# Optimization experiments

Measured on AMD Instinct MI355X. Metric: run time of the kernel, lower is better.

The kernel has to match this reference:

```python
import jax, jax.numpy as jnp
import numpy as np

B, IC, HC = 262144, 128, 128


def setup_inputs() -> dict:
    key = jax.random.key(0)
    ks = jax.random.split(key, 12)
    s_ih = 1.0 / np.sqrt(IC)
    s_hh = 1.0 / np.sqrt(HC)
    return {
        "x": jax.random.normal(ks[0], (B, IC), jnp.float32),
        "u": jax.random.uniform(ks[1], (B, 1), jnp.float32),
        "h": jax.random.normal(ks[2], (B, HC), jnp.float32) * 0.1,
        "c": jax.random.normal(ks[3], (B, HC), jnp.float32) * 0.1,
        "delta_u": jax.random.uniform(ks[4], (B, 1), jnp.float32),
        "skip": jax.random.randint(ks[5], (B,), 0, 2) == 1,
        # LSTMCell params (PyTorch gate order: i, f, g, o)
        "W_ih": jax.random.normal(ks[6], (4 * HC, IC), jnp.float32) * s_ih,
        "W_hh": jax.random.normal(ks[7], (4 * HC, HC), jnp.float32) * s_hh,
        "b_ih": jnp.zeros((4 * HC,), jnp.float32),
        "b_hh": jnp.zeros((4 * HC,), jnp.float32),
        # Linear(hc -> 1), bias initialized to 1 per the module
        "lin_w": jax.random.normal(ks[8], (1, HC), jnp.float32) * s_hh,
        "lin_b": jnp.ones((1,), jnp.float32),
    }


def _ste_round(u):
    # straight-through estimator: forward round, identity backward
    return u + jax.lax.stop_gradient(jnp.round(u) - u)


def reference(x, u, h, c, delta_u, skip, W_ih, W_hh, b_ih, b_hh, lin_w, lin_b):
    bu = _ste_round(u)  # [B,1]

    # --- no-skip branch: LSTM cell + update-gate linear ---
    gates = x @ W_ih.T + b_ih + h @ W_hh.T + b_hh  # [B,4*HC]
    i, f, g, o = jnp.split(gates, 4, axis=1)
    i = jax.nn.sigmoid(i)
    f = jax.nn.sigmoid(f)
    g = jnp.tanh(g)
    o = jax.nn.sigmoid(o)
    nc = f * c + i * g
    nh = o * jnp.tanh(nc)
    new_h_n = nh * bu
    new_c_n = nc * bu
    delta_u_n = jax.nn.sigmoid(new_c_n @ lin_w.T + lin_b)  # [B,1]
    new_u_n = delta_u_n * bu

    # --- skip branch: decay state, accumulate u ---
    keep = 1.0 - bu
    new_h_s = h * keep
    new_c_s = c * keep
    new_u_s = jnp.clip(u + delta_u, 0.0, 1.0) * keep

    # --- recombine by skip mask (equivalent to the gather/scatter routing) ---
    sk = skip[:, None]
    new_u = jnp.where(sk, new_u_s, new_u_n)
    new_h = jnp.where(sk, new_h_s, new_h_n)
    new_c = jnp.where(sk, new_c_s, new_c_n)
    d_u = jnp.where(sk, delta_u, delta_u_n)

    n_skips_after = jnp.ceil(0.5 / new_u) - 1.0
    return new_u, (new_h, new_c), d_u, n_skips_after
```

## Files before the change

### kernel.cpp

```cpp
#include <hip/hip_runtime.h>


typedef _Float16 half8  __attribute__((ext_vector_type(8)));
typedef _Float16 half4v __attribute__((ext_vector_type(4)));
typedef float    float4v __attribute__((ext_vector_type(4)));

#define B_ROWS 262144
#define TM 64
#define XPITCH 264
#define XPLANE (TM * XPITCH)
#define WCOMP  131072

__device__ __forceinline__ float sigmoidf_(float v) { return 1.0f / (1.0f + __expf(-v)); }
__device__ __forceinline__ float tanhf_(float v) {
    float ax = fabsf(v);
    float t = __expf(-2.0f * ax);
    float r = (1.0f - t) / (1.0f + t);
    return copysignf(r, v);
}

__global__ void prep_kernel(const float* __restrict__ W_ih, const float* __restrict__ W_hh,
                            const float* __restrict__ b_ih, const float* __restrict__ b_hh,
                            _Float16* __restrict__ Wp, float* __restrict__ bias,
                            int* __restrict__ counter) {
    if (blockIdx.x == 0 && threadIdx.x == 0) *counter = 0;
    int idx = blockIdx.x * 256 + threadIdx.x;
    int n = idx >> 8, k = idx & 255;
    float v = (k < 128) ? W_ih[n * 128 + k] : W_hh[n * 128 + (k - 128)];
    _Float16 wh = (_Float16)v;
    _Float16 wl = (_Float16)(v - (float)wh);
    int kb = k >> 5, quad = (k >> 3) & 3, j = k & 7;
    int nt = n >> 4, n16 = n & 15, lane = quad * 16 + n16;
    int base = (kb * 32 + nt) * 512 + lane * 8 + j;
    Wp[base] = wh;
    Wp[WCOMP + base] = wl;
    if (idx < 512) bias[idx] = b_ih[idx] + b_hh[idx];
}

__global__ void classify_kernel(const float* __restrict__ u, const float* __restrict__ h,
                                const float* __restrict__ c, const float* __restrict__ delta_u,
                                const int* __restrict__ skip, const float* __restrict__ lin_b,
                                int* __restrict__ counter, int* __restrict__ act_idx,
                                float* __restrict__ out) {
    __shared__ int s_cat[TM];
    const int tid = threadIdx.x;
    const int m0  = blockIdx.x * TM;

    float* out_u  = out;
    float* out_h  = out + (size_t)B_ROWS;
    float* out_c  = out + (size_t)B_ROWS * 129;
    float* out_du = out + (size_t)B_ROWS * 257;
    float* out_ns = out + (size_t)B_ROWS * 258;

    if (tid < TM) {
        int row = m0 + tid;
        float uv  = u[row];
        float duv = delta_u[row];
        int   sk  = skip[row];
        float buv = rintf(uv);
        bool active = (sk == 0) && (buv != 0.0f);
        s_cat[tid] = active ? 2 : ((sk != 0 && buv == 0.0f) ? 1 : 0);

        if (!active) {
            float nu, duo;
            if (sk != 0) {
                nu  = (buv == 0.0f) ? fminf(fmaxf(uv + duv, 0.0f), 1.0f) : 0.0f;
                duo = duv;
            } else {
                nu  = 0.0f;
                duo = sigmoidf_(lin_b[0]);
            }
            float nsk = ceilf(0.5f / nu) - 1.0f;
            if (!__builtin_isfinite(nsk)) nsk = 1.0e30f;
            out_u[row]  = nu;
            out_du[row] = duo;
            out_ns[row] = nsk;
        }
        unsigned long long mask = __ballot(active);
        int nact = __popcll(mask);
        int base = 0;
        if (tid == 0 && nact) base = atomicAdd(counter, nact);
        base = __shfl(base, 0, 64);
        if (active) {
            int pos = __popcll(mask & ((1ull << tid) - 1ull));
            act_idx[base + pos] = row;
        }
    }
    __syncthreads();

    #pragma unroll
    for (int it = 0; it < 8; ++it) {
        int r = it * 8 + (tid >> 5);
        int cat = s_cat[r];
        if (cat == 2) continue;
        size_t m = (size_t)(m0 + r);
        int c4 = (tid & 31) * 4;
        float4v vh = {0.f, 0.f, 0.f, 0.f}, vc = {0.f, 0.f, 0.f, 0.f};
        if (cat == 1) {
            vh = *(const float4v*)&h[m * 128 + c4];
            vc = *(const float4v*)&c[m * 128 + c4];
        }
        *(float4v*)&out_h[m * 128 + c4] = vh;
        *(float4v*)&out_c[m * 128 + c4] = vc;
    }
}

__launch_bounds__(256, 2)
__global__ void gemm_kernel(const float* __restrict__ x, const float* __restrict__ h,
                            const float* __restrict__ c,
                            const float* __restrict__ lin_w, const float* __restrict__ lin_b,
                            const _Float16* __restrict__ Wp, const float* __restrict__ bias,
                            const int* __restrict__ counter, const int* __restrict__ act_idx,
                            float* __restrict__ out) {
    const int n_act = *counter;
    if ((int)blockIdx.x * TM >= n_act) return;

    __shared__ __align__(16) _Float16 Xs[2 * XPLANE];
    __shared__ float zw[4][TM];
    __shared__ int   s_rid[TM];

    const int tid = threadIdx.x;

    if (tid < TM) {
        int g = blockIdx.x * TM + tid;
        s_rid[tid] = act_idx[g < n_act ? g : n_act - 1];
    }
    __syncthreads();

    #pragma unroll
    for (int i = 0; i < 16; ++i) {
        int id2 = i * 256 + tid;
        int r = id2 >> 6, c4 = (id2 & 63) * 4;
        size_t srow = (size_t)s_rid[r];
        float4v v;
        if (c4 < 128) v = *(const float4v*)&x[srow * 128 + c4];
        else          v = *(const float4v*)&h[srow * 128 + (c4 - 128)];
        half4v hi, lo;
        #pragma unroll
        for (int e = 0; e < 4; ++e) {
            _Float16 hh = (_Float16)v[e];
            hi[e] = hh;
            lo[e] = (_Float16)(v[e] - (float)hh);
        }
        *(half4v*)&Xs[r * XPITCH + c4]          = hi;
        *(half4v*)&Xs[XPLANE + r * XPITCH + c4] = lo;
    }
    __syncthreads();

    const int lane = tid & 63, w = tid >> 6;
    const int n16 = lane & 15, quad = lane >> 4;

    int ntid[8];
    #pragma unroll
    for (int g = 0; g < 4; ++g)
        #pragma unroll
        for (int p = 0; p < 2; ++p) ntid[g * 2 + p] = w * 2 + g * 8 + p;

    float4v acc[8][4];
    #pragma unroll
    for (int t = 0; t < 8; ++t)
        #pragma unroll
        for (int mt = 0; mt < 4; ++mt) acc[t][mt] = (float4v){0.f, 0.f, 0.f, 0.f};

    #pragma unroll 1
    for (int kb = 0; kb < 8; ++kb) {
        half8 bh[8], bl[8];
        #pragma unroll
        for (int t = 0; t < 8; ++t) {
            const _Float16* bp = Wp + (size_t)(kb * 32 + ntid[t]) * 512 + lane * 8;
            bh[t] = *(const half8*)bp;
            bl[t] = *(const half8*)(bp + WCOMP);
        }
        half8 ah[4], al[4];
        const int koff = kb * 32 + quad * 8;
        #pragma unroll
        for (int mt = 0; mt < 4; ++mt) {
            int m = mt * 16 + n16;
            ah[mt] = *(const half8*)&Xs[m * XPITCH + koff];
            al[mt] = *(const half8*)&Xs[XPLANE + m * XPITCH + koff];
        }
        #pragma unroll
        for (int t = 0; t < 8; ++t)
            #pragma unroll
            for (int mt = 0; mt < 4; ++mt) {
                acc[t][mt] = __builtin_amdgcn_mfma_f32_16x16x32_f16(ah[mt], bh[t], acc[t][mt], 0, 0, 0);
                acc[t][mt] = __builtin_amdgcn_mfma_f32_16x16x32_f16(al[mt], bh[t], acc[t][mt], 0, 0, 0);
                acc[t][mt] = __builtin_amdgcn_mfma_f32_16x16x32_f16(ah[mt], bl[t], acc[t][mt], 0, 0, 0);
            }
    }

    float* out_u  = out;
    float* out_h  = out + (size_t)B_ROWS;
    float* out_c  = out + (size_t)B_ROWS * 129;
    float* out_du = out + (size_t)B_ROWS * 257;
    float* out_ns = out + (size_t)B_ROWS * 258;

    float zpart[4][4];
    #pragma unroll
    for (int mt = 0; mt < 4; ++mt)
        #pragma unroll
        for (int reg = 0; reg < 4; ++reg) zpart[mt][reg] = 0.f;

    #pragma unroll
    for (int p = 0; p < 2; ++p) {
        int hc = w * 32 + p * 16 + n16;
        float bi = bias[hc], bf = bias[hc + 128], bg = bias[hc + 256], bo = bias[hc + 384];
        float lw = lin_w[hc];
        #pragma unroll
        for (int mt = 0; mt < 4; ++mt) {
            #pragma unroll
            for (int reg = 0; reg < 4; ++reg) {
                int row = mt * 16 + quad * 4 + reg;
                bool valid = blockIdx.x * TM + row < n_act;
                size_t m = (size_t)s_rid[row];
                float iv = sigmoidf_(acc[0 * 2 + p][mt][reg] + bi);
                float fv = sigmoidf_(acc[1 * 2 + p][mt][reg] + bf);
                float gv = tanhf_  (acc[2 * 2 + p][mt][reg] + bg);
                float ov = sigmoidf_(acc[3 * 2 + p][mt][reg] + bo);
                float cin = c[m * 128 + hc];
                float ncv = fv * cin + iv * gv;
                float nhv = ov * tanhf_(ncv);
                if (valid) {
                    out_h[m * 128 + hc] = nhv;
                    out_c[m * 128 + hc] = ncv;
                }
                zpart[mt][reg] += ncv * lw;
            }
        }
    }

    #pragma unroll
    for (int mt = 0; mt < 4; ++mt)
        #pragma unroll
        for (int reg = 0; reg < 4; ++reg) {
            float v = zpart[mt][reg];
            v += __shfl_xor(v, 1, 64);
            v += __shfl_xor(v, 2, 64);
            v += __shfl_xor(v, 4, 64);
            v += __shfl_xor(v, 8, 64);
            if (n16 == 0) zw[w][mt * 16 + quad * 4 + reg] = v;
        }
    __syncthreads();

    if (tid < TM) {
        int row = tid;
        if (blockIdx.x * TM + row < n_act) {
            float z = zw[0][row] + zw[1][row] + zw[2][row] + zw[3][row];
            float dun = sigmoidf_(z + lin_b[0]);
            float nsk = ceilf(0.5f / dun) - 1.0f;
            if (!__builtin_isfinite(nsk)) nsk = 1.0e30f;
            size_t m = (size_t)s_rid[row];
            out_u[m]  = dun;
            out_du[m] = dun;
            out_ns[m] = nsk;
        }
    }
}

extern "C" void kernel_launch(void* const* d_in, const int* in_sizes, int n_in,
                              void* d_out, int out_size, void* d_ws, size_t ws_size,
                              hipStream_t stream) {
    const float* x     = (const float*)d_in[0];
    const float* u     = (const float*)d_in[1];
    const float* h     = (const float*)d_in[2];
    const float* c     = (const float*)d_in[3];
    const float* du    = (const float*)d_in[4];
    const int*   skip  = (const int*)d_in[5];
    const float* W_ih  = (const float*)d_in[6];
    const float* W_hh  = (const float*)d_in[7];
    const float* b_ih  = (const float*)d_in[8];
    const float* b_hh  = (const float*)d_in[9];
    const float* lin_w = (const float*)d_in[10];
    const float* lin_b = (const float*)d_in[11];
    float* outp = (float*)d_out;

    _Float16* Wp   = (_Float16*)d_ws;
    float* bias    = (float*)((char*)d_ws + 2 * WCOMP * sizeof(_Float16));
    int* counter   = (int*)((char*)d_ws + 2 * WCOMP * sizeof(_Float16) + 2048);
    int* act_idx   = (int*)((char*)d_ws + 2 * WCOMP * sizeof(_Float16) + 2048 + 64);

    prep_kernel<<<512, 256, 0, stream>>>(W_ih, W_hh, b_ih, b_hh, Wp, bias, counter);
    classify_kernel<<<B_ROWS / TM, 256, 0, stream>>>(u, h, c, du, skip, lin_b,
                                                     counter, act_idx, outp);
    gemm_kernel<<<B_ROWS / TM, 256, 0, stream>>>(x, h, c, lin_w, lin_b, Wp, bias,
                                                 counter, act_idx, outp);
}
```

Baseline: 616.5 us.

## Halve GEMM row tile and split K staging into two halves for occupancy

The gemm kernel's row tile goes from 64 to 32, and the shared-memory staging of the split-fp16 activations is done in two K halves (x then h), which shrinks LDS to about a quarter. Accumulator registers are halved and launch bounds are raised to 4 blocks per SM so more waves fit per CU. Weight fragments are now loaded per n-tile inside the inner loop rather than all up front. The cost is twice as many blocks, each re-reading the full weight matrix from cache, plus an extra barrier pair per block.

```diff
diff --git a/kernel.cpp b/kernel.cpp
--- a/kernel.cpp
+++ b/kernel.cpp
@@ -7,8 +7,9 @@
 
 #define B_ROWS 262144
 #define TM 64
-#define XPITCH 264
-#define XPLANE (TM * XPITCH)
+#define TG 32
+#define XPITCH_H 136
+#define XPLANE_H (TG * XPITCH_H)
 #define WCOMP  131072
 
 __device__ __forceinline__ float sigmoidf_(float v) { return 1.0f / (1.0f + __expf(-v)); }
@@ -105,7 +106,7 @@
     }
 }
 
-__launch_bounds__(256, 2)
+__launch_bounds__(256, 4)
 __global__ void gemm_kernel(const float* __restrict__ x, const float* __restrict__ h,
                             const float* __restrict__ c,
                             const float* __restrict__ lin_w, const float* __restrict__ lin_b,
@@ -113,37 +114,17 @@
                             const int* __restrict__ counter, const int* __restrict__ act_idx,
                             float* __restrict__ out) {
     const int n_act = *counter;
-    if ((int)blockIdx.x * TM >= n_act) return;
-
-    __shared__ __align__(16) _Float16 Xs[2 * XPLANE];
-    __shared__ float zw[4][TM];
-    __shared__ int   s_rid[TM];
+    if ((int)blockIdx.x * TG >= n_act) return;
+
+    __shared__ __align__(16) _Float16 Xs[2 * XPLANE_H];
+    __shared__ float zw[4][TG];
+    __shared__ int   s_rid[TG];
 
     const int tid = threadIdx.x;
 
-    if (tid < TM) {
-        int g = blockIdx.x * TM + tid;
+    if (tid < TG) {
+        int g = blockIdx.x * TG + tid;
         s_rid[tid] = act_idx[g < n_act ? g : n_act - 1];
-    }
-    __syncthreads();
-
-    #pragma unroll
-    for (int i = 0; i < 16; ++i) {
-        int id2 = i * 256 + tid;
-        int r = id2 >> 6, c4 = (id2 & 63) * 4;
-        size_t srow = (size_t)s_rid[r];
-        float4v v;
-        if (c4 < 128) v = *(const float4v*)&x[srow * 128 + c4];
-        else          v = *(const float4v*)&h[srow * 128 + (c4 - 128)];
-        half4v hi, lo;
-        #pragma unroll
-        for (int e = 0; e < 4; ++e) {
-            _Float16 hh = (_Float16)v[e];
-            hi[e] = hh;
-            lo[e] = (_Float16)(v[e] - (float)hh);
-        }
-        *(half4v*)&Xs[r * XPITCH + c4]          = hi;
-        *(half4v*)&Xs[XPLANE + r * XPITCH + c4] = lo;
     }
     __syncthreads();
 
@@ -156,37 +137,59 @@
         #pragma unroll
         for (int p = 0; p < 2; ++p) ntid[g * 2 + p] = w * 2 + g * 8 + p;
 
-    float4v acc[8][4];
+    float4v acc[8][2];
     #pragma unroll
     for (int t = 0; t < 8; ++t)
         #pragma unroll
-        for (int mt = 0; mt < 4; ++mt) acc[t][mt] = (float4v){0.f, 0.f, 0.f, 0.f};
+        for (int mt = 0; mt < 2; ++mt) acc[t][mt] = (float4v){0.f, 0.f, 0.f, 0.f};
 
     #pragma unroll 1
-    for (int kb = 0; kb < 8; ++kb) {
-        half8 bh[8], bl[8];
-        #pragma unroll
-        for (int t = 0; t < 8; ++t) {
-            const _Float16* bp = Wp + (size_t)(kb * 32 + ntid[t]) * 512 + lane * 8;
-            bh[t] = *(const half8*)bp;
-            bl[t] = *(const half8*)(bp + WCOMP);
-        }
-        half8 ah[4], al[4];
-        const int koff = kb * 32 + quad * 8;
-        #pragma unroll
-        for (int mt = 0; mt < 4; ++mt) {
-            int m = mt * 16 + n16;
-            ah[mt] = *(const half8*)&Xs[m * XPITCH + koff];
-            al[mt] = *(const half8*)&Xs[XPLANE + m * XPITCH + koff];
-        }
-        #pragma unroll
-        for (int t = 0; t < 8; ++t)
-            #pragma unroll
-            for (int mt = 0; mt < 4; ++mt) {
-                acc[t][mt] = __builtin_amdgcn_mfma_f32_16x16x32_f16(ah[mt], bh[t], acc[t][mt], 0, 0, 0);
-                acc[t][mt] = __builtin_amdgcn_mfma_f32_16x16x32_f16(al[mt], bh[t], acc[t][mt], 0, 0, 0);
-                acc[t][mt] = __builtin_amdgcn_mfma_f32_16x16x32_f16(ah[mt], bl[t], acc[t][mt], 0, 0, 0);
-            }
+    for (int kh = 0; kh < 2; ++kh) {
+        #pragma unroll
+        for (int i = 0; i < 4; ++i) {
+            int idx = i * 256 + tid;
+            int r = idx >> 5, c4 = (idx & 31) * 4;
+            size_t srow = (size_t)s_rid[r];
+            float4v v;
+            if (kh == 0) v = *(const float4v*)&x[srow * 128 + c4];
+            else         v = *(const float4v*)&h[srow * 128 + c4];
+            half4v hi, lo;
+            #pragma unroll
+            for (int e = 0; e < 4; ++e) {
+                _Float16 hh = (_Float16)v[e];
+                hi[e] = hh;
+                lo[e] = (_Float16)(v[e] - (float)hh);
+            }
+            *(half4v*)&Xs[r * XPITCH_H + c4]             = hi;
+            *(half4v*)&Xs[XPLANE_H + r * XPITCH_H + c4]  = lo;
+        }
+        __syncthreads();
+
+        #pragma unroll
+        for (int kbl = 0; kbl < 4; ++kbl) {
+            const int kbg = kh * 4 + kbl;
+            half8 ah[2], al[2];
+            const int koff = kbl * 32 + quad * 8;
+            #pragma unroll
+            for (int mt = 0; mt < 2; ++mt) {
+                int m = mt * 16 + n16;
+                ah[mt] = *(const half8*)&Xs[m * XPITCH_H + koff];
+                al[mt] = *(const half8*)&Xs[XPLANE_H + m * XPITCH_H + koff];
+            }
+            #pragma unroll
+            for (int t = 0; t < 8; ++t) {
+                const _Float16* bp = Wp + (size_t)(kbg * 32 + ntid[t]) * 512 + lane * 8;
+                half8 bh = *(const half8*)bp;
+                half8 bl = *(const half8*)(bp + WCOMP);
+                #pragma unroll
+                for (int mt = 0; mt < 2; ++mt) {
+                    acc[t][mt] = __builtin_amdgcn_mfma_f32_16x16x32_f16(ah[mt], bh, acc[t][mt], 0, 0, 0);
+                    acc[t][mt] = __builtin_amdgcn_mfma_f32_16x16x32_f16(al[mt], bh, acc[t][mt], 0, 0, 0);
+                    acc[t][mt] = __builtin_amdgcn_mfma_f32_16x16x32_f16(ah[mt], bl, acc[t][mt], 0, 0, 0);
+                }
+            }
+        }
+        __syncthreads();
     }
 
     float* out_u  = out;
@@ -195,9 +198,9 @@
     float* out_du = out + (size_t)B_ROWS * 257;
     float* out_ns = out + (size_t)B_ROWS * 258;
 
-    float zpart[4][4];
-    #pragma unroll
-    for (int mt = 0; mt < 4; ++mt)
+    float zpart[2][4];
+    #pragma unroll
+    for (int mt = 0; mt < 2; ++mt)
         #pragma unroll
         for (int reg = 0; reg < 4; ++reg) zpart[mt][reg] = 0.f;
 
@@ -207,11 +210,11 @@
         float bi = bias[hc], bf = bias[hc + 128], bg = bias[hc + 256], bo = bias[hc + 384];
         float lw = lin_w[hc];
         #pragma unroll
-        for (int mt = 0; mt < 4; ++mt) {
+        for (int mt = 0; mt < 2; ++mt) {
             #pragma unroll
             for (int reg = 0; reg < 4; ++reg) {
                 int row = mt * 16 + quad * 4 + reg;
-                bool valid = blockIdx.x * TM + row < n_act;
+                bool valid = blockIdx.x * TG + row < n_act;
                 size_t m = (size_t)s_rid[row];
                 float iv = sigmoidf_(acc[0 * 2 + p][mt][reg] + bi);
                 float fv = sigmoidf_(acc[1 * 2 + p][mt][reg] + bf);
@@ -230,7 +233,7 @@
     }
 
     #pragma unroll
-    for (int mt = 0; mt < 4; ++mt)
+    for (int mt = 0; mt < 2; ++mt)
         #pragma unroll
         for (int reg = 0; reg < 4; ++reg) {
             float v = zpart[mt][reg];
@@ -242,9 +245,9 @@
         }
     __syncthreads();
 
-    if (tid < TM) {
+    if (tid < TG) {
         int row = tid;
-        if (blockIdx.x * TM + row < n_act) {
+        if (blockIdx.x * TG + row < n_act) {
             float z = zw[0][row] + zw[1][row] + zw[2][row] + zw[3][row];
             float dun = sigmoidf_(z + lin_b[0]);
             float nsk = ceilf(0.5f / dun) - 1.0f;
@@ -282,6 +285,6 @@
     prep_kernel<<<512, 256, 0, stream>>>(W_ih, W_hh, b_ih, b_hh, Wp, bias, counter);
     classify_kernel<<<B_ROWS / TM, 256, 0, stream>>>(u, h, c, du, skip, lin_b,
                                                      counter, act_idx, outp);
-    gemm_kernel<<<B_ROWS / TM, 256, 0, stream>>>(x, h, c, lin_w, lin_b, Wp, bias,
+    gemm_kernel<<<B_ROWS / TG, 256, 0, stream>>>(x, h, c, lin_w, lin_b, Wp, bias,
                                                  counter, act_idx, outp);
 }
```

New measurement: 697.0 us. 13.1% more time.
